# Kernel tuning notes

Measured on AMD Instinct MI355X. Metric: run time of the kernel, lower is better.

## Reference

```python
import jax, jax.numpy as jnp
import numpy as np

N_NODES = 10000
N_EDGES = 320000
AVG_NEIGH = 32.0


def ssp(x):
    # ShiftedSoftPlus
    return jax.nn.softplus(x) - jnp.asarray(np.log(2.0), x.dtype)


def setup_inputs() -> dict:
    key = jax.random.key(0)
    ks = jax.random.split(key, 16)
    inp = {
        "node_feats0": jax.random.normal(ks[0], (N_NODES, 64), jnp.float32),
        "node_feats1": jax.random.normal(ks[1], (N_NODES, 64, 3), jnp.float32),
        "node_attrs": jax.random.uniform(ks[2], (N_NODES, 4), jnp.float32),
        "edge_embedding": jax.random.uniform(ks[3], (N_EDGES, 8), jnp.float32),
        "edge_attrs": jax.random.normal(ks[4], (N_EDGES, 4), jnp.float32),
        "edge_src": jax.random.randint(ks[5], (N_EDGES,), 0, N_NODES),
        "edge_dst": jax.random.randint(ks[6], (N_EDGES,), 0, N_NODES),
        "W1_0": jax.random.normal(ks[7], (64, 64), jnp.float32),
        "W1_1": jax.random.normal(ks[8], (64, 64), jnp.float32),
        "Wr1": jax.random.normal(ks[9], (8, 8), jnp.float32),
        "Wr2": jax.random.normal(ks[10], (8, 256), jnp.float32),
        "W2_0": jax.random.normal(ks[11], (128, 128), jnp.float32),
        "W2_1": jax.random.normal(ks[12], (128, 64), jnp.float32),
        "Wsc_0": jax.random.normal(ks[13], (64, 4, 128), jnp.float32),
        "Wsc_1": jax.random.normal(ks[14], (64, 4, 64), jnp.float32),
    }
    return inp


def _tfn_layer(node_feats0, node_feats1, node_attrs, edge_embedding, edge_attrs,
               edge_src, edge_dst, W1_0, W1_1, Wr1, Wr2, W2_0, W2_1, Wsc_0, Wsc_1):
    N = node_feats0.shape[0]
    # --- linear_1 (e3nn Linear: per-irrep block, 1/sqrt(fan_in)) ---
    x0 = (node_feats0 @ W1_0) / jnp.sqrt(64.0)                       # [N,64]
    x1 = jnp.einsum('nuc,uw->nwc', node_feats1, W1_1) / jnp.sqrt(64.0)  # [N,64,3]
    # --- radial MLP: 8 -> 8 (ssp) -> 256, no bias ---
    h = ssp(edge_embedding @ Wr1 / jnp.sqrt(8.0))
    w = (h @ Wr2 / jnp.sqrt(8.0)).reshape(-1, 4, 64)                  # [E,4,64]
    # --- gather source node features ---
    xs0 = x0[edge_src]                                                # [E,64]
    xs1 = x1[edge_src]                                                # [E,64,3]
    y0 = edge_attrs[:, 0:1]                                           # [E,1] (0e SH)
    y1 = edge_attrs[:, 1:4]                                           # [E,3] (1o SH)
    # --- per-edge equivariant tensor product (uvu, 4 instructions) ---
    m00 = w[:, 0] * xs0 * y0                                          # 0e x 0e -> 0e
    m01 = w[:, 1][:, :, None] * xs0[:, :, None] * y1[:, None, :]      # 0e x 1o -> 1o
    m10 = w[:, 2][:, :, None] * xs1 * y0[:, :, None]                  # 1o x 0e -> 1o
    m11 = w[:, 3] * jnp.einsum('euc,ec->eu', xs1, y1) / jnp.sqrt(3.0)  # 1o x 1o -> 0e
    mid0 = jnp.concatenate([m00, m11], axis=1)                        # [E,128]
    mid1 = jnp.concatenate([m01, m10], axis=1)                        # [E,128,3]
    # --- scatter-sum to destination nodes, / sqrt(avg_num_neighbors) ---
    agg0 = jax.ops.segment_sum(mid0, edge_dst, num_segments=N) / jnp.sqrt(AVG_NEIGH)
    agg1 = jax.ops.segment_sum(mid1, edge_dst, num_segments=N) / jnp.sqrt(AVG_NEIGH)
    # --- linear_2 to conv output irreps 128x0e + 64x1o ---
    out0 = (agg0 @ W2_0) / jnp.sqrt(128.0)                            # [N,128]
    out1 = jnp.einsum('nuc,uw->nwc', agg1, W2_1) / jnp.sqrt(128.0)    # [N,64,3]
    # --- self connection: FullyConnectedTensorProduct(node_feats_in, node_attrs) ---
    sc0 = jnp.einsum('nu,nv,uvw->nw', node_feats0, node_attrs, Wsc_0) / jnp.sqrt(256.0)
    sc1 = jnp.einsum('nuc,nv,uvw->nwc', node_feats1, node_attrs, Wsc_1) / jnp.sqrt(256.0)
    n0 = out0 + sc0
    n1 = out1 + sc1
    # --- Gate nonlinearity: 64 scalars (ssp), 64 gates (ssp) gating 64x1o ---
    scalars = ssp(n0[:, :64])
    gates = ssp(n0[:, 64:])
    gated = n1 * gates[:, :, None]
    # --- resnet ---
    new0 = node_feats0 + scalars
    new1 = node_feats1 + gated
    return jnp.concatenate([new0, new1.reshape(N, 192)], axis=1)      # [N,256]


def reference(node_feats0, node_feats1, node_attrs, edge_embedding, edge_attrs,
              edge_src, edge_dst, W1_0, W1_1, Wr1, Wr2, W2_0, W2_1, Wsc_0, Wsc_1):
    return _tfn_layer(node_feats0, node_feats1, node_attrs, edge_embedding, edge_attrs,
                      edge_src, edge_dst, W1_0, W1_1, Wr1, Wr2, W2_0, W2_1, Wsc_0, Wsc_1)
```

## Files before the change

kernel.cpp:

```cpp
#include <hip/hip_runtime.h>
#include <math.h>

#define N_NODES 10000
#define N_EDGES 320000
#define DEG_CAP 128

typedef short bf16x8 __attribute__((ext_vector_type(8)));
typedef float f32x4 __attribute__((ext_vector_type(4)));

__device__ __forceinline__ float ssp(float x) {
    float ax = fabsf(x);
    return fmaxf(x, 0.0f) + log1pf(expf(-ax)) - 0.69314718055994531f;
}
__device__ __forceinline__ float bcastf(float v, int l) {
    return __uint_as_float(__builtin_amdgcn_readlane(__float_as_uint(v), l));
}
__device__ __forceinline__ int bcasti(int v, int l) {
    return __builtin_amdgcn_readlane(v, l);
}
__device__ __forceinline__ int div3(int q) {
    return (q * 21846) >> 16;
}
__device__ __forceinline__ unsigned short f2bf(float f) {
    unsigned int u = __float_as_uint(f);
    u += 0x7fff + ((u >> 16) & 1);
    return (unsigned short)(u >> 16);
}


__global__ __launch_bounds__(256) void wprep_kernel(
    const float* __restrict__ W2_0, const float* __restrict__ Wsc0,
    const float* __restrict__ W2_1, const float* __restrict__ Wsc1,
    uint4* __restrict__ wb0, uint4* __restrict__ wb1)
{
    const int tid = blockIdx.x*256 + threadIdx.x;
    const float rs128 = 0.088388347648318447f;
    const float s16 = 0.0625f;
    if (tid < 6144) {
        const int kstep = tid >> 9;
        const int rem = tid & 511;
        const int col = ((rem >> 6) << 4) + (rem & 15);
        const int kb = kstep*32 + (((rem & 63) >> 4) << 3);
        unsigned int u[4];
        #pragma unroll
        for (int h = 0; h < 4; ++h) {
            const int k0 = kb + 2*h, k1 = k0 + 1;
            const float f0 = (k0 < 128) ? W2_0[k0*128+col]*rs128 : Wsc0[(k0-128)*128+col]*s16;
            const float f1 = (k1 < 128) ? W2_0[k1*128+col]*rs128 : Wsc0[(k1-128)*128+col]*s16;
            u[h] = (unsigned int)f2bf(f0) | ((unsigned int)f2bf(f1) << 16);
        }
        wb0[tid] = make_uint4(u[0], u[1], u[2], u[3]);
    } else if (tid < 9216) {
        const int t2 = tid - 6144;
        const int kstep = t2 >> 8;
        const int rem = t2 & 255;
        const int col = ((rem >> 6) << 4) + (rem & 15);
        const int kb = kstep*32 + (((rem & 63) >> 4) << 3);
        unsigned int u[4];
        #pragma unroll
        for (int h = 0; h < 4; ++h) {
            const int k0 = kb + 2*h, k1 = k0 + 1;
            const float f0 = (k0 < 128) ? W2_1[k0*64+col]*rs128 : Wsc1[(k0-128)*64+col]*s16;
            const float f1 = (k1 < 128) ? W2_1[k1*64+col]*rs128 : Wsc1[(k1-128)*64+col]*s16;
            u[h] = (unsigned int)f2bf(f0) | ((unsigned int)f2bf(f1) << 16);
        }
        wb1[t2] = make_uint4(u[0], u[1], u[2], u[3]);
    }
}


__global__ __launch_bounds__(256) void node_pre_kernel(
        const float* __restrict__ nf0, const float* __restrict__ nf1,
        const float* __restrict__ W1_0, const float* __restrict__ W1_1,
        const int* __restrict__ edst, int* __restrict__ counts, int* __restrict__ csr,
        uint2* __restrict__ xpack) {
    const int n = blockIdx.x;
    const int t = threadIdx.x;
    __shared__ float s_f0[64];
    __shared__ float s_f1[192];
    __shared__ unsigned short sx[4][64];
    if (t < 64) s_f0[t] = nf0[n*64 + t];
    else        s_f1[t-64] = nf1[n*192 + (t-64)];
    if (t >= 224) {
        int e = n*32 + (t - 224);
        int d = edst[e];
        int p = atomicAdd(&counts[d], 1);
        if (p < DEG_CAP) csr[d * DEG_CAP + p] = e;
    }
    __syncthreads();
    if (t < 64) {
        float acc = 0.f;
        #pragma unroll 8
        for (int u = 0; u < 64; ++u) acc += s_f0[u] * W1_0[u*64 + t];
        sx[0][t] = f2bf(acc * 0.125f);
    } else {
        const int c = (t - 64) >> 6;
        const int w = t & 63;
        float acc = 0.f;
        #pragma unroll 8
        for (int u = 0; u < 64; ++u) acc += s_f1[u*3 + c] * W1_1[u*64 + w];
        sx[1+c][w] = f2bf(acc * 0.125f);
    }
    __syncthreads();
    if (t < 64) {
        uint2 v;
        v.x = (unsigned int)sx[0][t] | ((unsigned int)sx[1][t] << 16);
        v.y = (unsigned int)sx[2][t] | ((unsigned int)sx[3][t] << 16);
        xpack[(size_t)n*64 + t] = v;
    }
}


__global__ __launch_bounds__(256) void edge_kernel(
    const float* __restrict__ eemb, const float* __restrict__ eattr,
    const int* __restrict__ esrc,
    const int* __restrict__ counts, const int* __restrict__ csr,
    const uint2* __restrict__ xpack,
    const float* __restrict__ Wr1, const float* __restrict__ Wr2,
    unsigned int* __restrict__ agg0p, unsigned int* __restrict__ agg1p)
{
    const int wid = threadIdx.x >> 6;
    const int nl  = wid >> 1;
    const int p   = wid & 1;
    const int n   = blockIdx.x * 2 + nl;
    const int u   = threadIdx.x & 63;
    const int j8  = u & 7;

    const float rs8 = 0.35355339059327373f;
    const float rs3 = 0.57735026918962576f;

    float wr2[4][8];
    #pragma unroll
    for (int k = 0; k < 4; ++k) {
        #pragma unroll
        for (int j = 0; j < 8; ++j) {
            float v = Wr2[j*256 + k*64 + u] * rs8;
            wr2[k][j] = (k == 3) ? v * rs3 : v;
        }
    }
    float wr1c[8];
    #pragma unroll
    for (int i = 0; i < 8; ++i) wr1c[i] = Wr1[i*8 + j8] * rs8;

    float A[8] = {0.f,0.f,0.f,0.f,0.f,0.f,0.f,0.f};

    const int craw = counts[n];
    const int cnt  = craw < DEG_CAP ? craw : DEG_CAP;
    const int base0 = n * DEG_CAP;

    int e = 0, src = 0;
    {
        const int b0 = p*8;
        if (b0 < cnt) {
            const int m0 = cnt - b0 < 8 ? cnt - b0 : 8;
            const int s0 = (u >> 3) < m0 ? (u >> 3) : 0;
            e = csr[base0 + b0 + s0];
            src = esrc[e];
        }
    }

    for (int b = p*8; b < cnt; b += 16) {
        const int e_cur = e, src_cur = src;
        const int m = cnt - b < 8 ? cnt - b : 8;
        const int bn = b + 16;
        if (bn < cnt) {
            const int mn = cnt - bn < 8 ? cnt - bn : 8;
            const int sn = (u >> 3) < mn ? (u >> 3) : 0;
            e = csr[base0 + bn + sn];
            src = esrc[e];
        }

        const float4 e0 = *reinterpret_cast<const float4*>(eemb + (size_t)e_cur*8);
        const float4 e1 = *reinterpret_cast<const float4*>(eemb + (size_t)e_cur*8 + 4);
        float pre = e0.x*wr1c[0] + e0.y*wr1c[1] + e0.z*wr1c[2] + e0.w*wr1c[3]
                  + e1.x*wr1c[4] + e1.y*wr1c[5] + e1.z*wr1c[6] + e1.w*wr1c[7];
        const float h  = ssp(pre);
        const float yl = eattr[(size_t)e_cur*4 + (j8 & 3)];

        uint2 g[8];
        #pragma unroll
        for (int s = 0; s < 8; ++s) {
            const int ssrc = bcasti(src_cur, s*8);
            g[s] = xpack[(size_t)ssrc*64 + u];
        }

        #pragma unroll
        for (int s = 0; s < 8; ++s) {
            if (s >= m) break;
            const int bs = s * 8;
            const float xs0 = __uint_as_float(g[s].x << 16);
            const float x1a = __uint_as_float(g[s].x & 0xffff0000u);
            const float x1b = __uint_as_float(g[s].y << 16);
            const float x1c = __uint_as_float(g[s].y & 0xffff0000u);
            float w0 = 0.f, w1 = 0.f, w2 = 0.f, w3 = 0.f;
            #pragma unroll
            for (int j = 0; j < 8; ++j) {
                const float hj = bcastf(h, bs + j);
                w0 += hj * wr2[0][j];
                w1 += hj * wr2[1][j];
                w2 += hj * wr2[2][j];
                w3 += hj * wr2[3][j];
            }
            const float y0 = bcastf(yl, bs+0);
            const float y1 = bcastf(yl, bs+1);
            const float y2 = bcastf(yl, bs+2);
            const float y3 = bcastf(yl, bs+3);
            A[0] += w0 * xs0 * y0;
            const float t01 = w1 * xs0;
            A[1] += t01*y1; A[2] += t01*y2; A[3] += t01*y3;
            const float t10 = w2 * y0;
            A[4] += t10*x1a; A[5] += t10*x1b; A[6] += t10*x1c;
            A[7] += w3 * (x1a*y1 + x1b*y2 + x1c*y3);
        }
    }

    __shared__ float red[2][2][8][64];
    #pragma unroll
    for (int a = 0; a < 8; ++a) red[nl][p][a][u] = A[a];
    __syncthreads();

    const float rs32 = 0.17677669529663687f;
    if (threadIdx.x < 128) {
        const int nlq = threadIdx.x >> 6;
        const int kp  = threadIdx.x & 63;
        const int a   = (kp < 32) ? 0 : 7;
        const int uu0 = (kp < 32) ? 2*kp : 2*kp - 64;
        const float v0 = (red[nlq][0][a][uu0]   + red[nlq][1][a][uu0])   * rs32;
        const float v1 = (red[nlq][0][a][uu0+1] + red[nlq][1][a][uu0+1]) * rs32;
        const int nn = blockIdx.x*2 + nlq;
        agg0p[(size_t)nn*64 + kp] = (unsigned int)f2bf(v0) | ((unsigned int)f2bf(v1) << 16);
    }
    #pragma unroll
    for (int it = 0; it < 2; ++it) {
        const int idx = it*256 + threadIdx.x;
        if (idx < 384) {
            const int nlq = (idx >= 192) ? 1 : 0;
            const int pi  = idx - nlq*192;
            const int c   = pi >> 6, kp = pi & 63;
            const int a   = (kp < 32) ? (1+c) : (4+c);
            const int u0  = (kp < 32) ? (2*kp) : (2*kp - 64);
            const float v0 = (red[nlq][0][a][u0]   + red[nlq][1][a][u0])   * rs32;
            const float v1 = (red[nlq][0][a][u0+1] + red[nlq][1][a][u0+1]) * rs32;
            const int nn = blockIdx.x*2 + nlq;
            agg1p[(size_t)nn*192 + pi] = (unsigned int)f2bf(v0) | ((unsigned int)f2bf(v1) << 16);
        }
    }
}


__global__ __launch_bounds__(512) void epiA_mfma_kernel(
    const float* __restrict__ nf0, const float* __restrict__ nattr,
    const unsigned int* __restrict__ agg0p, const uint4* __restrict__ wb0,
    float* __restrict__ out, float* __restrict__ gbuf)
{
    __shared__ unsigned int sA[3072];
    const int t = threadIdx.x;
    const int node0 = blockIdx.x * 16;

    #pragma unroll
    for (int it = 0; it < 6; ++it) {
        int idx = it*512 + t;
        int q = idx >> 6;
        int row = div3(q);
        int seg = q - 3*row;
        int kp = seg*64 + (idx & 63);
        int node = node0 + row;
        unsigned int val;
        if (kp < 64) val = agg0p[(size_t)node*64 + kp];
        else {
            int pk = kp - 64;
            float f = nf0[(size_t)node*64 + (pk >> 1)];
            const float2 at = *reinterpret_cast<const float2*>(nattr + (size_t)node*4 + ((pk & 1) << 1));
            val = (unsigned int)f2bf(f*at.x) | ((unsigned int)f2bf(f*at.y) << 16);
        }
        sA[row*192 + (kp ^ ((row & 7) << 2))] = val;
    }
    __syncthreads();

    const int ct = t >> 6;
    const int lane = t & 63;
    const int m = lane & 15;
    const int ks = lane >> 4;
    const char* sab = reinterpret_cast<const char*>(sA) + m*768;
    const int swz = (m & 7) << 4;

    f32x4 acc = {0.f, 0.f, 0.f, 0.f};
    #pragma unroll
    for (int kstep = 0; kstep < 12; ++kstep) {
        bf16x8 a = *reinterpret_cast<const bf16x8*>(sab + (((kstep << 6) + (ks << 4)) ^ swz));
        bf16x8 b = *reinterpret_cast<const bf16x8*>(wb0 + (kstep << 9) + (ct << 6) + lane);
        acc = __builtin_amdgcn_mfma_f32_16x16x32_bf16(a, b, acc, 0, 0, 0);
    }

    const int col = ct*16 + m;
    #pragma unroll
    for (int q = 0; q < 4; ++q) {
        const int node = node0 + ks*4 + q;
        const float v = ssp(acc[q]);
        if (col < 64) out[(size_t)node*256 + col] = nf0[(size_t)node*64 + col] + v;
        else          gbuf[(size_t)node*64 + (col - 64)] = v;
    }
}


__global__ __launch_bounds__(256) void epiB_mfma_kernel(
    const float* __restrict__ nf1, const float* __restrict__ nattr,
    const unsigned int* __restrict__ agg1p, const uint4* __restrict__ wb1,
    const float* __restrict__ gbuf, float* __restrict__ out)
{
    __shared__ unsigned int sB[3072];
    const int t = threadIdx.x;
    const int row0 = blockIdx.x * 16;

    #pragma unroll
    for (int it = 0; it < 12; ++it) {
        int idx = it*256 + t;
        int q = idx >> 6;
        int row = div3(q);
        int seg = q - 3*row;
        int kp = seg*64 + (idx & 63);
        int r = row0 + row;
        int n = div3(r);
        int c = r - 3*n;
        unsigned int val;
        if (kp < 64) val = agg1p[(size_t)n*192 + c*64 + kp];
        else {
            int pk = kp - 64;
            float f = nf1[(size_t)n*192 + (pk >> 1)*3 + c];
            const float2 at = *reinterpret_cast<const float2*>(nattr + (size_t)n*4 + ((pk & 1) << 1));
            val = (unsigned int)f2bf(f*at.x) | ((unsigned int)f2bf(f*at.y) << 16);
        }
        sB[row*192 + (kp ^ ((row & 7) << 2))] = val;
    }
    __syncthreads();

    const int ct = t >> 6;
    const int lane = t & 63;
    const int m = lane & 15;
    const int ks = lane >> 4;
    const char* sab = reinterpret_cast<const char*>(sB) + m*768;
    const int swz = (m & 7) << 4;

    f32x4 acc = {0.f, 0.f, 0.f, 0.f};
    #pragma unroll
    for (int kstep = 0; kstep < 12; ++kstep) {
        bf16x8 a = *reinterpret_cast<const bf16x8*>(sab + (((kstep << 6) + (ks << 4)) ^ swz));
        bf16x8 b = *reinterpret_cast<const bf16x8*>(wb1 + (kstep << 8) + (ct << 6) + lane);
        acc = __builtin_amdgcn_mfma_f32_16x16x32_bf16(a, b, acc, 0, 0, 0);
    }

    const int col = ct*16 + m;
    #pragma unroll
    for (int q = 0; q < 4; ++q) {
        const int r = row0 + ks*4 + q;
        const int n = div3(r);
        const int c = r - 3*n;
        const float g = gbuf[(size_t)n*64 + col];
        out[(size_t)n*256 + 64 + col*3 + c] = nf1[(size_t)n*192 + col*3 + c] + acc[q]*g;
    }
}


extern "C" void kernel_launch(void* const* d_in, const int* in_sizes, int n_in,
                              void* d_out, int out_size, void* d_ws, size_t ws_size,
                              hipStream_t stream) {
    const float* nf0   = (const float*)d_in[0];
    const float* nf1   = (const float*)d_in[1];
    const float* nattr = (const float*)d_in[2];
    const float* eemb  = (const float*)d_in[3];
    const float* eattr = (const float*)d_in[4];
    const int*   esrc  = (const int*)d_in[5];
    const int*   edst  = (const int*)d_in[6];
    const float* W1_0  = (const float*)d_in[7];
    const float* W1_1  = (const float*)d_in[8];
    const float* Wr1   = (const float*)d_in[9];
    const float* Wr2   = (const float*)d_in[10];
    const float* W2_0  = (const float*)d_in[11];
    const float* W2_1  = (const float*)d_in[12];
    const float* Wsc0  = (const float*)d_in[13];
    const float* Wsc1  = (const float*)d_in[14];
    float* out = (float*)d_out;

    char* ws = (char*)d_ws;
    uint2* xpack = (uint2*)ws;         ws += (size_t)N_NODES*64*sizeof(uint2);
    int* counts  = (int*)ws;           ws += (size_t)N_NODES*sizeof(int);
    int* csr2    = (int*)ws;           ws += (size_t)N_NODES*DEG_CAP*sizeof(int);
    unsigned int* agg0p = (unsigned int*)ws;
                                       ws += (size_t)N_NODES*64*sizeof(unsigned int);
    unsigned int* agg1p = (unsigned int*)ws;
                                       ws += (size_t)N_NODES*192*sizeof(unsigned int);
    float* gbuf  = (float*)ws;         ws += (size_t)N_NODES*64*sizeof(float);
    uint4* wb0   = (uint4*)ws;         ws += (size_t)6144*sizeof(uint4);
    uint4* wb1   = (uint4*)ws;         ws += (size_t)3072*sizeof(uint4);

    hipMemsetAsync(counts, 0, N_NODES*sizeof(int), stream);
    wprep_kernel<<<36, 256, 0, stream>>>(W2_0, Wsc0, W2_1, Wsc1, wb0, wb1);
    node_pre_kernel<<<N_NODES, 256, 0, stream>>>(nf0, nf1, W1_0, W1_1, edst, counts, csr2, xpack);
    edge_kernel<<<(N_NODES+1)/2, 256, 0, stream>>>(eemb, eattr, esrc, counts, csr2,
        xpack, Wr1, Wr2, agg0p, agg1p);
    epiA_mfma_kernel<<<N_NODES/16, 512, 0, stream>>>(nf0, nattr, agg0p, wb0, out, gbuf);
    epiB_mfma_kernel<<<(3*N_NODES)/16, 256, 0, stream>>>(nf1, nattr, agg1p, wb1, gbuf, out);
}
```

Measured before the change: 133.3 us.

## Store src in CSR and prefetch edge data and gathers one iteration ahead

The CSR build now stores (edge, src) pairs, so the edge kernel no longer has to chase esrc[e] through a dependent load. The edge loop is software-pipelined: embeddings, attributes and xpack gathers for the next 8-edge batch are issued before the current batch is computed, to hide gather latency. DEG_CAP drops to 96 and gbuf reuses the CSR buffer to save workspace. The cost is higher register pressure from double-buffered gather data. The lower cap also risks dropping edges for any node whose in-degree exceeds 96.

```diff
diff --git a/kernel.cpp b/kernel.cpp
--- a/kernel.cpp
+++ b/kernel.cpp
@@ -3,7 +3,7 @@
 
 #define N_NODES 10000
 #define N_EDGES 320000
-#define DEG_CAP 128
+#define DEG_CAP 96
 
 typedef short bf16x8 __attribute__((ext_vector_type(8)));
 typedef float f32x4 __attribute__((ext_vector_type(4)));
@@ -72,7 +72,8 @@
 __global__ __launch_bounds__(256) void node_pre_kernel(
         const float* __restrict__ nf0, const float* __restrict__ nf1,
         const float* __restrict__ W1_0, const float* __restrict__ W1_1,
-        const int* __restrict__ edst, int* __restrict__ counts, int* __restrict__ csr,
+        const int* __restrict__ edst, const int* __restrict__ esrc,
+        int* __restrict__ counts, int2* __restrict__ csr2,
         uint2* __restrict__ xpack) {
     const int n = blockIdx.x;
     const int t = threadIdx.x;
@@ -84,8 +85,9 @@
     if (t >= 224) {
         int e = n*32 + (t - 224);
         int d = edst[e];
+        int sv = esrc[e];
         int p = atomicAdd(&counts[d], 1);
-        if (p < DEG_CAP) csr[d * DEG_CAP + p] = e;
+        if (p < DEG_CAP) csr2[d * DEG_CAP + p] = make_int2(e, sv);
     }
     __syncthreads();
     if (t < 64) {
@@ -113,8 +115,7 @@
 
 __global__ __launch_bounds__(256) void edge_kernel(
     const float* __restrict__ eemb, const float* __restrict__ eattr,
-    const int* __restrict__ esrc,
-    const int* __restrict__ counts, const int* __restrict__ csr,
+    const int* __restrict__ counts, const int2* __restrict__ csr2,
     const uint2* __restrict__ xpack,
     const float* __restrict__ Wr1, const float* __restrict__ Wr2,
     unsigned int* __restrict__ agg0p, unsigned int* __restrict__ agg1p)
@@ -148,50 +149,65 @@
     const int cnt  = craw < DEG_CAP ? craw : DEG_CAP;
     const int base0 = n * DEG_CAP;
 
-    int e = 0, src = 0;
-    {
-        const int b0 = p*8;
-        if (b0 < cnt) {
-            const int m0 = cnt - b0 < 8 ? cnt - b0 : 8;
-            const int s0 = (u >> 3) < m0 ? (u >> 3) : 0;
-            e = csr[base0 + b0 + s0];
-            src = esrc[e];
-        }
-    }
-
-    for (int b = p*8; b < cnt; b += 16) {
-        const int e_cur = e, src_cur = src;
+    int2 es = make_int2(0, 0);
+    float4 m0 = {0,0,0,0}, m1 = {0,0,0,0};
+    float yy = 0.f;
+    uint2 g[8];
+    #pragma unroll
+    for (int s = 0; s < 8; ++s) g[s] = make_uint2(0u, 0u);
+
+    const int b0 = p*8;
+    if (b0 < cnt) {
+        const int mm = cnt - b0 < 8 ? cnt - b0 : 8;
+        const int sl = (u >> 3) < mm ? (u >> 3) : 0;
+        es = csr2[base0 + b0 + sl];
+        m0 = *reinterpret_cast<const float4*>(eemb + (size_t)es.x*8);
+        m1 = *reinterpret_cast<const float4*>(eemb + (size_t)es.x*8 + 4);
+        yy = eattr[(size_t)es.x*4 + (j8 & 3)];
+        #pragma unroll
+        for (int s = 0; s < 8; ++s)
+            g[s] = xpack[(size_t)bcasti(es.y, s*8)*64 + u];
+    }
+
+    for (int b = b0; b < cnt; b += 16) {
         const int m = cnt - b < 8 ? cnt - b : 8;
+        const float4 cm0 = m0, cm1 = m1;
+        const float cy = yy;
+        uint2 cg[8];
+        #pragma unroll
+        for (int s = 0; s < 8; ++s) cg[s] = g[s];
+
         const int bn = b + 16;
-        if (bn < cnt) {
+        const bool more = (bn < cnt);
+        int2 esn = make_int2(0, 0);
+        if (more) {
             const int mn = cnt - bn < 8 ? cnt - bn : 8;
             const int sn = (u >> 3) < mn ? (u >> 3) : 0;
-            e = csr[base0 + bn + sn];
-            src = esrc[e];
-        }
-
-        const float4 e0 = *reinterpret_cast<const float4*>(eemb + (size_t)e_cur*8);
-        const float4 e1 = *reinterpret_cast<const float4*>(eemb + (size_t)e_cur*8 + 4);
-        float pre = e0.x*wr1c[0] + e0.y*wr1c[1] + e0.z*wr1c[2] + e0.w*wr1c[3]
-                  + e1.x*wr1c[4] + e1.y*wr1c[5] + e1.z*wr1c[6] + e1.w*wr1c[7];
-        const float h  = ssp(pre);
-        const float yl = eattr[(size_t)e_cur*4 + (j8 & 3)];
-
-        uint2 g[8];
-        #pragma unroll
-        for (int s = 0; s < 8; ++s) {
-            const int ssrc = bcasti(src_cur, s*8);
-            g[s] = xpack[(size_t)ssrc*64 + u];
+            esn = csr2[base0 + bn + sn];
+        }
+
+        float pre = cm0.x*wr1c[0] + cm0.y*wr1c[1] + cm0.z*wr1c[2] + cm0.w*wr1c[3]
+                  + cm1.x*wr1c[4] + cm1.y*wr1c[5] + cm1.z*wr1c[6] + cm1.w*wr1c[7];
+        const float h = ssp(pre);
+
+        if (more) {
+            es = esn;
+            m0 = *reinterpret_cast<const float4*>(eemb + (size_t)es.x*8);
+            m1 = *reinterpret_cast<const float4*>(eemb + (size_t)es.x*8 + 4);
+            yy = eattr[(size_t)es.x*4 + (j8 & 3)];
+            #pragma unroll
+            for (int s = 0; s < 8; ++s)
+                g[s] = xpack[(size_t)bcasti(es.y, s*8)*64 + u];
         }
 
         #pragma unroll
         for (int s = 0; s < 8; ++s) {
             if (s >= m) break;
             const int bs = s * 8;
-            const float xs0 = __uint_as_float(g[s].x << 16);
-            const float x1a = __uint_as_float(g[s].x & 0xffff0000u);
-            const float x1b = __uint_as_float(g[s].y << 16);
-            const float x1c = __uint_as_float(g[s].y & 0xffff0000u);
+            const float xs0 = __uint_as_float(cg[s].x << 16);
+            const float x1a = __uint_as_float(cg[s].x & 0xffff0000u);
+            const float x1b = __uint_as_float(cg[s].y << 16);
+            const float x1c = __uint_as_float(cg[s].y & 0xffff0000u);
             float w0 = 0.f, w1 = 0.f, w2 = 0.f, w3 = 0.f;
             #pragma unroll
             for (int j = 0; j < 8; ++j) {
@@ -201,10 +217,10 @@
                 w2 += hj * wr2[2][j];
                 w3 += hj * wr2[3][j];
             }
-            const float y0 = bcastf(yl, bs+0);
-            const float y1 = bcastf(yl, bs+1);
-            const float y2 = bcastf(yl, bs+2);
-            const float y3 = bcastf(yl, bs+3);
+            const float y0 = bcastf(cy, bs+0);
+            const float y1 = bcastf(cy, bs+1);
+            const float y2 = bcastf(cy, bs+2);
+            const float y3 = bcastf(cy, bs+3);
             A[0] += w0 * xs0 * y0;
             const float t01 = w1 * xs0;
             A[1] += t01*y1; A[2] += t01*y2; A[3] += t01*y3;
@@ -384,19 +400,20 @@
     char* ws = (char*)d_ws;
     uint2* xpack = (uint2*)ws;         ws += (size_t)N_NODES*64*sizeof(uint2);
     int* counts  = (int*)ws;           ws += (size_t)N_NODES*sizeof(int);
-    int* csr2    = (int*)ws;           ws += (size_t)N_NODES*DEG_CAP*sizeof(int);
+    int2* csr2   = (int2*)ws;          ws += (size_t)N_NODES*DEG_CAP*sizeof(int2);
     unsigned int* agg0p = (unsigned int*)ws;
                                        ws += (size_t)N_NODES*64*sizeof(unsigned int);
     unsigned int* agg1p = (unsigned int*)ws;
                                        ws += (size_t)N_NODES*192*sizeof(unsigned int);
-    float* gbuf  = (float*)ws;         ws += (size_t)N_NODES*64*sizeof(float);
     uint4* wb0   = (uint4*)ws;         ws += (size_t)6144*sizeof(uint4);
     uint4* wb1   = (uint4*)ws;         ws += (size_t)3072*sizeof(uint4);
+    float* gbuf  = (float*)csr2;
 
     hipMemsetAsync(counts, 0, N_NODES*sizeof(int), stream);
     wprep_kernel<<<36, 256, 0, stream>>>(W2_0, Wsc0, W2_1, Wsc1, wb0, wb1);
-    node_pre_kernel<<<N_NODES, 256, 0, stream>>>(nf0, nf1, W1_0, W1_1, edst, counts, csr2, xpack);
-    edge_kernel<<<(N_NODES+1)/2, 256, 0, stream>>>(eemb, eattr, esrc, counts, csr2,
+    node_pre_kernel<<<N_NODES, 256, 0, stream>>>(nf0, nf1, W1_0, W1_1, edst, esrc,
+        counts, csr2, xpack);
+    edge_kernel<<<(N_NODES+1)/2, 256, 0, stream>>>(eemb, eattr, counts, csr2,
         xpack, Wr1, Wr2, agg0p, agg1p);
     epiA_mfma_kernel<<<N_NODES/16, 512, 0, stream>>>(nf0, nattr, agg0p, wb0, out, gbuf);
     epiB_mfma_kernel<<<(3*N_NODES)/16, 256, 0, stream>>>(nf1, nattr, agg1p, wb1, gbuf, out);
```

New measurement: 130.7 us. -2.0%, faster.
